# Kernel optimization log

Measured on AMD Instinct MI355X. Metric: run time of the kernel, lower is better.

The kernel has to match this reference:

```python
import jax, jax.numpy as jnp
import numpy as np

DIM = 1024
DEPTH = 6
HEADS = 16
MLP = 4096
HEAD_DIM = DIM // HEADS
SCALE = HEAD_DIM ** -0.5
EPS = 1e-5


def _ln(x, g, b):
    m = jnp.mean(x, axis=-1, keepdims=True)
    v = jnp.mean(jnp.square(x - m), axis=-1, keepdims=True)
    return (x - m) * jax.lax.rsqrt(v + EPS) * g + b


def setup_inputs() -> dict:
    key = jax.random.key(0)
    ks = jax.random.split(key, 16)
    B, N = 4, 1024
    s_d = 1.0 / np.sqrt(DIM)
    s_m = 1.0 / np.sqrt(MLP)
    inp = {
        "x1": jax.random.normal(ks[0], (B, N, DIM), jnp.float32),
        "x2": jax.random.normal(ks[1], (B, N, DIM), jnp.float32),
        # stacked per-layer params; Linear weights stored as [in, out]
        "ln1_g": jnp.ones((DEPTH, DIM), jnp.float32),
        "ln1_b": jnp.zeros((DEPTH, DIM), jnp.float32),
        "wq": jax.random.normal(ks[2], (DEPTH, DIM, DIM), jnp.float32) * s_d,
        "wk": jax.random.normal(ks[3], (DEPTH, DIM, DIM), jnp.float32) * s_d,
        "wv": jax.random.normal(ks[4], (DEPTH, DIM, DIM), jnp.float32) * s_d,
        "wo": jax.random.normal(ks[5], (DEPTH, DIM, DIM), jnp.float32) * s_d,
        "bo": jnp.zeros((DEPTH, DIM), jnp.float32),
        "ln2_g": jnp.ones((DEPTH, DIM), jnp.float32),
        "ln2_b": jnp.zeros((DEPTH, DIM), jnp.float32),
        "w1": jax.random.normal(ks[6], (DEPTH, DIM, MLP), jnp.float32) * s_d,
        "b1": jnp.zeros((DEPTH, MLP), jnp.float32),
        "w2": jax.random.normal(ks[7], (DEPTH, MLP, DIM), jnp.float32) * s_m,
        "b2": jnp.zeros((DEPTH, DIM), jnp.float32),
    }
    return inp


def _split_heads(t):
    b, n, _ = t.shape
    return t.reshape(b, n, HEADS, HEAD_DIM).transpose(0, 2, 1, 3)  # b h n d


def reference(x1, x2, ln1_g, ln1_b, wq, wk, wv, wo, bo, ln2_g, ln2_b, w1, b1, w2, b2):
    # dropout disabled (eval mode)
    for i in range(DEPTH):
        # PreNorm(MCA): same LayerNorm params applied to x1 and x2
        n1 = _ln(x1, ln1_g[i], ln1_b[i])
        n2 = _ln(x2, ln1_g[i], ln1_b[i])
        q = _split_heads(n1 @ wq[i])
        k = _split_heads(n2 @ wk[i])
        v = _split_heads(n2 @ wv[i])
        dots = jnp.einsum('bhqd,bhkd->bhqk', q, k) * SCALE
        attn = jax.nn.softmax(dots, axis=-1)
        out = jnp.einsum('bhqk,bhkd->bhqd', attn, v)
        b, h, n, d = out.shape
        out = out.transpose(0, 2, 1, 3).reshape(b, n, h * d)
        x1 = out @ wo[i] + bo[i] + x1
        # PreNorm(FeedForward)
        nf = _ln(x1, ln2_g[i], ln2_b[i])
        hdn = jax.nn.gelu(nf @ w1[i] + b1[i], approximate=False)
        x1 = hdn @ w2[i] + b2[i] + x1
    return x1
```

## Files before the change

### kernel.cpp

```cpp
#include <hip/hip_runtime.h>
#include <stdint.h>

#define N_SEQ 1024
#define N_TOK 4096
#define ATT_SCALE 0.125f

typedef unsigned short u16;
typedef __attribute__((ext_vector_type(8))) short short8;
typedef __attribute__((ext_vector_type(4))) short short4v;
typedef __attribute__((ext_vector_type(4))) float f32x4;

__device__ __forceinline__ u16 f2bf(float f) {
  uint32_t u = __float_as_uint(f);
  u += 0x7fffu + ((u >> 16) & 1u);
  return (u16)(u >> 16);
}

__device__ __forceinline__ void gload16(const void* g, void* lds) {
  __builtin_amdgcn_global_load_lds(
      (const __attribute__((address_space(1))) unsigned int*)g,
      (__attribute__((address_space(3))) unsigned int*)lds, 16, 0, 0);
}

__global__ void copy_f32_kernel(const float* __restrict__ in, float* __restrict__ out) {
  int i = blockIdx.x * 256 + threadIdx.x;
  ((float4*)out)[i] = ((const float4*)in)[i];
}

__global__ __launch_bounds__(256) void tconv_kernel(const float* __restrict__ src,
                                                    u16* __restrict__ dst,
                                                    int K, int NN, size_t dstLS) {
  __shared__ u16 tile[64][68];
  int n0 = blockIdx.x * 64, k0 = blockIdx.y * 64, L = blockIdx.z;
  const float* s = src + (size_t)L * K * NN;
  u16* d = dst + (size_t)L * dstLS;
  int t = threadIdx.x;
  int rr = t >> 4, cc = (t & 15) * 4;
#pragma unroll
  for (int ii = 0; ii < 4; ii++) {
    int kl = rr + ii * 16;
    float4 v = *(const float4*)&s[(size_t)(k0 + kl) * NN + n0 + cc];
    tile[cc + 0][kl] = f2bf(v.x);
    tile[cc + 1][kl] = f2bf(v.y);
    tile[cc + 2][kl] = f2bf(v.z);
    tile[cc + 3][kl] = f2bf(v.w);
  }
  __syncthreads();
#pragma unroll
  for (int ii = 0; ii < 4; ii++) {
    int nl = rr + ii * 16;
    short4v o;
    o.x = (short)tile[nl][cc + 0];
    o.y = (short)tile[nl][cc + 1];
    o.z = (short)tile[nl][cc + 2];
    o.w = (short)tile[nl][cc + 3];
    *(short4v*)&d[(size_t)(n0 + nl) * K + k0 + cc] = o;
  }
}

__global__ __launch_bounds__(256) void ln_kernel(const float* __restrict__ x,
                                                 const float* __restrict__ g,
                                                 const float* __restrict__ b,
                                                 u16* __restrict__ out) {
  int row = blockIdx.x;
  const float* xr = x + (size_t)row * 1024;
  int t = threadIdx.x;
  float4 v = *(const float4*)&xr[t * 4];
  float s = v.x + v.y + v.z + v.w;
  float sq = v.x * v.x + v.y * v.y + v.z * v.z + v.w * v.w;
#pragma unroll
  for (int m = 1; m < 64; m <<= 1) {
    s += __shfl_xor(s, m, 64);
    sq += __shfl_xor(sq, m, 64);
  }
  __shared__ float ps[8];
  int w = t >> 6;
  if ((t & 63) == 0) { ps[w] = s; ps[4 + w] = sq; }
  __syncthreads();
  s = ps[0] + ps[1] + ps[2] + ps[3];
  sq = ps[4] + ps[5] + ps[6] + ps[7];
  float mean = s * (1.0f / 1024.0f);
  float var = sq * (1.0f / 1024.0f) - mean * mean;
  float rs = rsqrtf(var + 1e-5f);
  float4 gv = *(const float4*)&g[t * 4];
  float4 bv = *(const float4*)&b[t * 4];
  short4v o;
  o.x = (short)f2bf((v.x - mean) * rs * gv.x + bv.x);
  o.y = (short)f2bf((v.y - mean) * rs * gv.y + bv.y);
  o.z = (short)f2bf((v.z - mean) * rs * gv.z + bv.z);
  o.w = (short)f2bf((v.w - mean) * rs * gv.w + bv.w);
  *(short4v*)&out[(size_t)row * 1024 + t * 4] = o;
}

template <int BM, int BN, int WM, int WN, int BK, int D, int MODE>
__global__ __launch_bounds__(WM * WN * 64, 2) void gemmP(const u16* __restrict__ A,
                                                         const u16* __restrict__ Bt,
                                                         u16* __restrict__ outb,
                                                         float* __restrict__ outf,
                                                         const float* __restrict__ bias,
                                                         const float* __restrict__ resid,
                                                         int N, int K) {
  static_assert(BK == 64, "swizzle assumes 8 x 16B chunks per row");
  constexpr int NW = WM * WN;
  constexpr int T = NW * 64;
  constexpr int WTM = BM / WM, WTN = BN / WN;
  constexpr int FM = WTM / 16, FN = WTN / 16;
  constexpr int AT = BM * BK, BTL = BN * BK;
  constexpr int LA = AT / 8 / T, LB = BTL / 8 / T;
  constexpr int LTOT = LA + LB;
  constexpr int WAITN = (D - 1) * LTOT;
  __shared__ u16 smem[D * (AT + BTL)];

  int t = threadIdx.x, lane = t & 63, w = t >> 6;
  int wm = w / WN, wn = w % WN;
  const u16* Ag = A + (size_t)(blockIdx.y * BM) * K;
  const u16* Bg = Bt + (size_t)(blockIdx.x * BN) * K;
  f32x4 acc[FM][FN] = {};

  auto stage = [&](int d, int k0) {
    u16* ab = smem + d * (AT + BTL);
    u16* bb = ab + AT;
#pragma unroll
    for (int l = 0; l < LA; l++) {
      int c = (l * NW + w) * 64 + lane;
      int r = c >> 3, s = c & 7;
      gload16(Ag + (size_t)r * K + k0 + ((s ^ (r & 7)) << 3), ab + (l * NW + w) * 512);
    }
#pragma unroll
    for (int l = 0; l < LB; l++) {
      int c = (l * NW + w) * 64 + lane;
      int r = c >> 3, s = c & 7;
      gload16(Bg + (size_t)r * K + k0 + ((s ^ (r & 7)) << 3), bb + (l * NW + w) * 512);
    }
  };

  const int NT = K / BK;
#pragma unroll
  for (int d = 0; d < D; d++) stage(d, d * BK);
  __builtin_amdgcn_sched_barrier(0);

  int buf = 0;
  for (int tt = 0; tt < NT; tt++) {
    asm volatile("s_waitcnt vmcnt(%0)" ::"n"(WAITN) : "memory");
    __builtin_amdgcn_s_barrier();
    __builtin_amdgcn_sched_barrier(0);
    const u16* ab = smem + buf * (AT + BTL);
    const u16* bb = ab + AT;
    short8 af[2][FM], bfr[2][FN];
#pragma unroll
    for (int ks = 0; ks < 2; ks++) {
      int j = ks * 4 + (lane >> 4);
#pragma unroll
      for (int mi = 0; mi < FM; mi++) {
        int rr = wm * WTM + mi * 16 + (lane & 15);
        af[ks][mi] = *(const short8*)&ab[rr * BK + ((j ^ (rr & 7)) << 3)];
      }
#pragma unroll
      for (int ni = 0; ni < FN; ni++) {
        int rr = wn * WTN + ni * 16 + (lane & 15);
        bfr[ks][ni] = *(const short8*)&bb[rr * BK + ((j ^ (rr & 7)) << 3)];
      }
    }
    asm volatile("s_waitcnt lgkmcnt(0)" ::: "memory");
    __builtin_amdgcn_sched_barrier(0);
    __builtin_amdgcn_s_barrier();
    __builtin_amdgcn_sched_barrier(0);
    stage(buf, ((tt + D) % NT) * BK);
    __builtin_amdgcn_sched_barrier(0);
#pragma unroll
    for (int ks = 0; ks < 2; ks++)
#pragma unroll
      for (int mi = 0; mi < FM; mi++)
#pragma unroll
        for (int ni = 0; ni < FN; ni++)
          acc[mi][ni] = __builtin_amdgcn_mfma_f32_16x16x32_bf16(af[ks][mi], bfr[ks][ni],
                                                                acc[mi][ni], 0, 0, 0);
    buf = (buf + 1 == D) ? 0 : buf + 1;
  }

  int r0 = blockIdx.y * BM + wm * WTM + ((lane >> 4) << 2);
  int c0 = blockIdx.x * BN + wn * WTN + (lane & 15);
#pragma unroll
  for (int mi = 0; mi < FM; mi++) {
#pragma unroll
    for (int r = 0; r < 4; r++) {
      size_t row = (size_t)(r0 + mi * 16 + r);
#pragma unroll
      for (int ni = 0; ni < FN; ni++) {
        size_t col = (size_t)(c0 + ni * 16);
        size_t idx = row * N + col;
        float val = acc[mi][ni][r];
        if (MODE == 0) {
          outb[idx] = f2bf(val);
        } else if (MODE == 1) {
          outf[idx] = val + bias[col] + resid[idx];
        } else {
          float xg = val + bias[col];
          outb[idx] = f2bf(0.5f * xg * (1.0f + erff(xg * 0.70710678f)));
        }
      }
    }
  }
}

__global__ __launch_bounds__(256) void attn_kernel(const u16* __restrict__ qb,
                                                   const u16* __restrict__ kvb,
                                                   u16* __restrict__ ob) {
  int qt = blockIdx.x, bh = blockIdx.y;
  int b = bh >> 4, h = bh & 15;
  int t = threadIdx.x, lane = t & 63, w = t >> 6;
  __shared__ u16 Qs[64 * 64];
  __shared__ u16 Ks[64 * 64];
  __shared__ u16 Vt[64 * 64];
  __shared__ u16 Ps[4][16 * 64];

  const u16* qbase = qb + (size_t)b * N_SEQ * 1024 + h * 64;
  const u16* kbase = kvb + (size_t)b * N_SEQ * 2048 + h * 64;
  const u16* vbase = kbase + 1024;
  u16* obase = ob + (size_t)b * N_SEQ * 1024 + h * 64;

  {
    int r = t >> 2, c = (t & 3) * 16;
    const u16* src = qbase + (size_t)(qt * 64 + r) * 1024 + c;
    *(short8*)&Qs[r * 64 + c] = *(const short8*)src;
    *(short8*)&Qs[r * 64 + c + 8] = *(const short8*)(src + 8);
  }
  __syncthreads();
  short8 qa0 = *(const short8*)&Qs[(w * 16 + (lane & 15)) * 64 + (lane >> 4) * 8];
  short8 qa1 = *(const short8*)&Qs[(w * 16 + (lane & 15)) * 64 + 32 + (lane >> 4) * 8];

  f32x4 o[4] = {};
  float m_r[4] = {-1e30f, -1e30f, -1e30f, -1e30f};
  float l_r[4] = {0.0f, 0.0f, 0.0f, 0.0f};

  for (int kt = 0; kt < 16; kt++) {
    __syncthreads();
    {
      int r = t >> 2, c = (t & 3) * 16;
      const u16* ksrc = kbase + (size_t)(kt * 64 + r) * 2048 + c;
      *(short8*)&Ks[r * 64 + c] = *(const short8*)ksrc;
      *(short8*)&Ks[r * 64 + c + 8] = *(const short8*)(ksrc + 8);
      const u16* vsrc = vbase + (size_t)(kt * 64 + r) * 2048 + c;
      short8 v0 = *(const short8*)vsrc;
      short8 v1 = *(const short8*)(vsrc + 8);
#pragma unroll
      for (int j = 0; j < 8; j++) {
        Vt[(c + j) * 64 + r] = (u16)v0[j];
        Vt[(c + 8 + j) * 64 + r] = (u16)v1[j];
      }
    }
    __syncthreads();

    f32x4 s[4] = {};
#pragma unroll
    for (int kb = 0; kb < 4; kb++) {
      short8 k0 = *(const short8*)&Ks[(kb * 16 + (lane & 15)) * 64 + (lane >> 4) * 8];
      short8 k1 = *(const short8*)&Ks[(kb * 16 + (lane & 15)) * 64 + 32 + (lane >> 4) * 8];
      s[kb] = __builtin_amdgcn_mfma_f32_16x16x32_bf16(qa0, k0, s[kb], 0, 0, 0);
      s[kb] = __builtin_amdgcn_mfma_f32_16x16x32_bf16(qa1, k1, s[kb], 0, 0, 0);
    }
    float fac[4], rowsum[4];
#pragma unroll
    for (int r = 0; r < 4; r++) {
      float a = fmaxf(fmaxf(s[0][r], s[1][r]), fmaxf(s[2][r], s[3][r])) * ATT_SCALE;
      a = fmaxf(a, __shfl_xor(a, 1, 64));
      a = fmaxf(a, __shfl_xor(a, 2, 64));
      a = fmaxf(a, __shfl_xor(a, 4, 64));
      a = fmaxf(a, __shfl_xor(a, 8, 64));
      float mn = fmaxf(m_r[r], a);
      fac[r] = __expf(m_r[r] - mn);
      m_r[r] = mn;
      rowsum[r] = 0.0f;
    }
#pragma unroll
    for (int kb = 0; kb < 4; kb++) {
#pragma unroll
      for (int r = 0; r < 4; r++) {
        float p = __expf(s[kb][r] * ATT_SCALE - m_r[r]);
        rowsum[r] += p;
        Ps[w][((lane >> 4) * 4 + r) * 64 + kb * 16 + (lane & 15)] = f2bf(p);
      }
    }
#pragma unroll
    for (int r = 0; r < 4; r++) {
      float rs = rowsum[r];
      rs += __shfl_xor(rs, 1, 64);
      rs += __shfl_xor(rs, 2, 64);
      rs += __shfl_xor(rs, 4, 64);
      rs += __shfl_xor(rs, 8, 64);
      l_r[r] = l_r[r] * fac[r] + rs;
      o[0][r] *= fac[r];
      o[1][r] *= fac[r];
      o[2][r] *= fac[r];
      o[3][r] *= fac[r];
    }
    __syncthreads();
#pragma unroll
    for (int ks = 0; ks < 2; ks++) {
      short8 pf = *(const short8*)&Ps[w][(lane & 15) * 64 + ks * 32 + (lane >> 4) * 8];
#pragma unroll
      for (int db = 0; db < 4; db++) {
        short8 vf = *(const short8*)&Vt[(db * 16 + (lane & 15)) * 64 + ks * 32 + (lane >> 4) * 8];
        o[db] = __builtin_amdgcn_mfma_f32_16x16x32_bf16(pf, vf, o[db], 0, 0, 0);
      }
    }
  }
#pragma unroll
  for (int r = 0; r < 4; r++) {
    float inv = 1.0f / l_r[r];
    size_t row = (size_t)(qt * 64 + w * 16 + (lane >> 4) * 4 + r);
#pragma unroll
    for (int db = 0; db < 4; db++)
      obase[row * 1024 + db * 16 + (lane & 15)] = f2bf(o[db][r] * inv);
  }
}

extern "C" void kernel_launch(void* const* d_in, const int* in_sizes, int n_in,
                              void* d_out, int out_size, void* d_ws, size_t ws_size,
                              hipStream_t stream) {
  const float* x1 = (const float*)d_in[0];
  const float* x2 = (const float*)d_in[1];
  const float* ln1_g = (const float*)d_in[2];
  const float* ln1_b = (const float*)d_in[3];
  const float* wq = (const float*)d_in[4];
  const float* wk = (const float*)d_in[5];
  const float* wv = (const float*)d_in[6];
  const float* wo = (const float*)d_in[7];
  const float* bo = (const float*)d_in[8];
  const float* ln2_g = (const float*)d_in[9];
  const float* ln2_b = (const float*)d_in[10];
  const float* w1 = (const float*)d_in[11];
  const float* b1 = (const float*)d_in[12];
  const float* w2 = (const float*)d_in[13];
  const float* b2 = (const float*)d_in[14];
  float* xout = (float*)d_out;

  u16* p = (u16*)d_ws;
  u16* wqt = p;  p += (size_t)6 * 1024 * 1024;
  u16* kvt = p;  p += (size_t)6 * 2048 * 1024;
  u16* wot = p;  p += (size_t)6 * 1024 * 1024;
  u16* w1t = p;  p += (size_t)6 * 4096 * 1024;
  u16* w2t = p;  p += (size_t)6 * 1024 * 4096;
  u16* n1 = p;   p += (size_t)N_TOK * 1024;
  u16* n2 = p;   p += (size_t)N_TOK * 1024;
  u16* qbuf = p; p += (size_t)N_TOK * 1024;
  u16* kvbuf = p; p += (size_t)N_TOK * 2048;
  u16* ao = p;   p += (size_t)N_TOK * 1024;
  u16* hid = p;  p += (size_t)N_TOK * 4096;

  dim3 blk(256);
  tconv_kernel<<<dim3(16, 16, 6), blk, 0, stream>>>(wq, wqt, 1024, 1024, (size_t)1024 * 1024);
  tconv_kernel<<<dim3(16, 16, 6), blk, 0, stream>>>(wk, kvt, 1024, 1024, (size_t)2048 * 1024);
  tconv_kernel<<<dim3(16, 16, 6), blk, 0, stream>>>(wv, kvt + (size_t)1024 * 1024, 1024, 1024, (size_t)2048 * 1024);
  tconv_kernel<<<dim3(16, 16, 6), blk, 0, stream>>>(wo, wot, 1024, 1024, (size_t)1024 * 1024);
  tconv_kernel<<<dim3(64, 16, 6), blk, 0, stream>>>(w1, w1t, 1024, 4096, (size_t)4096 * 1024);
  tconv_kernel<<<dim3(16, 64, 6), blk, 0, stream>>>(w2, w2t, 4096, 1024, (size_t)1024 * 4096);
  copy_f32_kernel<<<4096, blk, 0, stream>>>(x1, xout);

  for (int i = 0; i < 6; i++) {
    ln_kernel<<<N_TOK, blk, 0, stream>>>(xout, ln1_g + i * 1024, ln1_b + i * 1024, n1);
    ln_kernel<<<N_TOK, blk, 0, stream>>>(x2, ln1_g + i * 1024, ln1_b + i * 1024, n2);
    gemmP<128, 128, 4, 2, 64, 3, 0><<<dim3(8, 32), dim3(512), 0, stream>>>(
        n1, wqt + (size_t)i * 1024 * 1024, qbuf, nullptr, nullptr, nullptr, 1024, 1024);
    gemmP<128, 128, 2, 2, 64, 2, 0><<<dim3(16, 32), dim3(256), 0, stream>>>(
        n2, kvt + (size_t)i * 2048 * 1024, kvbuf, nullptr, nullptr, nullptr, 2048, 1024);
    attn_kernel<<<dim3(16, 64), blk, 0, stream>>>(qbuf, kvbuf, ao);
    gemmP<128, 128, 4, 2, 64, 3, 1><<<dim3(8, 32), dim3(512), 0, stream>>>(
        ao, wot + (size_t)i * 1024 * 1024, nullptr, xout, bo + i * 1024, xout, 1024, 1024);
    ln_kernel<<<N_TOK, blk, 0, stream>>>(xout, ln2_g + i * 1024, ln2_b + i * 1024, n1);
    gemmP<128, 128, 2, 2, 64, 2, 2><<<dim3(32, 32), dim3(256), 0, stream>>>(
        n1, w1t + (size_t)i * 4096 * 1024, hid, nullptr, b1 + i * 4096, nullptr, 4096, 1024);
    gemmP<128, 128, 4, 2, 64, 3, 1><<<dim3(8, 32), dim3(512), 0, stream>>>(
        hid, w2t + (size_t)i * 1024 * 4096, nullptr, xout, b2 + i * 1024, xout, 1024, 4096);
  }
}
```

Baseline: 1.721 ms.

## Interleave LDS fragment reads with MFMA in fixed double-buffered GEMM

Replaces the configurable-depth GEMM with a fixed two-stage double-buffered kernel. Within each K tile, LDS fragment reads are split into halves and interleaved with MFMA groups, using partial lgkmcnt waits and s_setprio to raise priority during matrix ops. Part of the math now runs after the next global-to-LDS stage is issued. Launch configs also change: most GEMMs drop to 4 waves, and the FFN-up GEMM uses 256x256 tiles with 8 waves. This trades prefetch depth and occupancy for better overlap of LDS latency with compute, and adds register pressure.

```diff
diff --git a/kernel.cpp b/kernel.cpp
--- a/kernel.cpp
+++ b/kernel.cpp
@@ -92,24 +92,23 @@
   *(short4v*)&out[(size_t)row * 1024 + t * 4] = o;
 }
 
-template <int BM, int BN, int WM, int WN, int BK, int D, int MODE>
-__global__ __launch_bounds__(WM * WN * 64, 2) void gemmP(const u16* __restrict__ A,
+template <int BM, int BN, int WM, int WN, int MODE>
+__global__ __launch_bounds__(WM * WN * 64, 2) void gemm8(const u16* __restrict__ A,
                                                          const u16* __restrict__ Bt,
                                                          u16* __restrict__ outb,
                                                          float* __restrict__ outf,
                                                          const float* __restrict__ bias,
                                                          const float* __restrict__ resid,
                                                          int N, int K) {
-  static_assert(BK == 64, "swizzle assumes 8 x 16B chunks per row");
+  constexpr int BK = 64;
   constexpr int NW = WM * WN;
   constexpr int T = NW * 64;
   constexpr int WTM = BM / WM, WTN = BN / WN;
-  constexpr int FM = WTM / 16, FN = WTN / 16;
+  constexpr int FM = WTM / 16, FN = WTN / 16, HM = FM / 2;
   constexpr int AT = BM * BK, BTL = BN * BK;
   constexpr int LA = AT / 8 / T, LB = BTL / 8 / T;
   constexpr int LTOT = LA + LB;
-  constexpr int WAITN = (D - 1) * LTOT;
-  __shared__ u16 smem[D * (AT + BTL)];
+  __shared__ u16 smem[2 * (AT + BTL)];
 
   int t = threadIdx.x, lane = t & 63, w = t >> 6;
   int wm = w / WN, wn = w % WN;
@@ -134,48 +133,83 @@
     }
   };
 
+  auto rdA = [&](const u16* ab, int mi, int ks) {
+    int rr = wm * WTM + mi * 16 + (lane & 15);
+    int j = ks * 4 + (lane >> 4);
+    return *(const short8*)&ab[rr * BK + ((j ^ (rr & 7)) << 3)];
+  };
+  auto rdB = [&](const u16* bb, int ni, int ks) {
+    int rr = wn * WTN + ni * 16 + (lane & 15);
+    int j = ks * 4 + (lane >> 4);
+    return *(const short8*)&bb[rr * BK + ((j ^ (rr & 7)) << 3)];
+  };
+
   const int NT = K / BK;
-#pragma unroll
-  for (int d = 0; d < D; d++) stage(d, d * BK);
+  stage(0, 0);
+  stage(1, BK);
   __builtin_amdgcn_sched_barrier(0);
 
   int buf = 0;
   for (int tt = 0; tt < NT; tt++) {
-    asm volatile("s_waitcnt vmcnt(%0)" ::"n"(WAITN) : "memory");
+    asm volatile("s_waitcnt vmcnt(%0)" ::"n"(LTOT) : "memory");
     __builtin_amdgcn_s_barrier();
     __builtin_amdgcn_sched_barrier(0);
     const u16* ab = smem + buf * (AT + BTL);
     const u16* bb = ab + AT;
-    short8 af[2][FM], bfr[2][FN];
-#pragma unroll
-    for (int ks = 0; ks < 2; ks++) {
-      int j = ks * 4 + (lane >> 4);
-#pragma unroll
-      for (int mi = 0; mi < FM; mi++) {
-        int rr = wm * WTM + mi * 16 + (lane & 15);
-        af[ks][mi] = *(const short8*)&ab[rr * BK + ((j ^ (rr & 7)) << 3)];
-      }
-#pragma unroll
-      for (int ni = 0; ni < FN; ni++) {
-        int rr = wn * WTN + ni * 16 + (lane & 15);
-        bfr[ks][ni] = *(const short8*)&bb[rr * BK + ((j ^ (rr & 7)) << 3)];
-      }
-    }
+    short8 b0[FN], a0lo[HM], a0hi[HM], b1[FN], a1lo[HM], a1hi[HM];
+#pragma unroll
+    for (int n = 0; n < FN; n++) b0[n] = rdB(bb, n, 0);
+#pragma unroll
+    for (int m = 0; m < HM; m++) a0lo[m] = rdA(ab, m, 0);
+#pragma unroll
+    for (int m = 0; m < HM; m++) a0hi[m] = rdA(ab, HM + m, 0);
+    asm volatile("s_waitcnt lgkmcnt(%0)" ::"n"(HM) : "memory");
+    __builtin_amdgcn_sched_barrier(0);
+#pragma unroll
+    for (int n = 0; n < FN; n++) b1[n] = rdB(bb, n, 1);
+#pragma unroll
+    for (int m = 0; m < HM; m++) a1lo[m] = rdA(ab, m, 1);
+    __builtin_amdgcn_s_setprio(1);
+#pragma unroll
+    for (int m = 0; m < HM; m++)
+#pragma unroll
+      for (int n = 0; n < FN; n++)
+        acc[m][n] = __builtin_amdgcn_mfma_f32_16x16x32_bf16(a0lo[m], b0[n], acc[m][n], 0, 0, 0);
+    __builtin_amdgcn_s_setprio(0);
+    asm volatile("s_waitcnt lgkmcnt(%0)" ::"n"(FN + HM) : "memory");
+    __builtin_amdgcn_sched_barrier(0);
+#pragma unroll
+    for (int m = 0; m < HM; m++) a1hi[m] = rdA(ab, HM + m, 1);
+    __builtin_amdgcn_s_setprio(1);
+#pragma unroll
+    for (int m = 0; m < HM; m++)
+#pragma unroll
+      for (int n = 0; n < FN; n++)
+        acc[HM + m][n] = __builtin_amdgcn_mfma_f32_16x16x32_bf16(a0hi[m], b0[n], acc[HM + m][n], 0, 0, 0);
+    __builtin_amdgcn_s_setprio(0);
+    asm volatile("s_waitcnt lgkmcnt(%0)" ::"n"(HM) : "memory");
+    __builtin_amdgcn_sched_barrier(0);
+    __builtin_amdgcn_s_setprio(1);
+#pragma unroll
+    for (int m = 0; m < HM; m++)
+#pragma unroll
+      for (int n = 0; n < FN; n++)
+        acc[m][n] = __builtin_amdgcn_mfma_f32_16x16x32_bf16(a1lo[m], b1[n], acc[m][n], 0, 0, 0);
+    __builtin_amdgcn_s_setprio(0);
     asm volatile("s_waitcnt lgkmcnt(0)" ::: "memory");
     __builtin_amdgcn_sched_barrier(0);
     __builtin_amdgcn_s_barrier();
     __builtin_amdgcn_sched_barrier(0);
-    stage(buf, ((tt + D) % NT) * BK);
-    __builtin_amdgcn_sched_barrier(0);
-#pragma unroll
-    for (int ks = 0; ks < 2; ks++)
-#pragma unroll
-      for (int mi = 0; mi < FM; mi++)
-#pragma unroll
-        for (int ni = 0; ni < FN; ni++)
-          acc[mi][ni] = __builtin_amdgcn_mfma_f32_16x16x32_bf16(af[ks][mi], bfr[ks][ni],
-                                                                acc[mi][ni], 0, 0, 0);
-    buf = (buf + 1 == D) ? 0 : buf + 1;
+    stage(buf, ((tt + 2) % NT) * BK);
+    __builtin_amdgcn_sched_barrier(0);
+    __builtin_amdgcn_s_setprio(1);
+#pragma unroll
+    for (int m = 0; m < HM; m++)
+#pragma unroll
+      for (int n = 0; n < FN; n++)
+        acc[HM + m][n] = __builtin_amdgcn_mfma_f32_16x16x32_bf16(a1hi[m], b1[n], acc[HM + m][n], 0, 0, 0);
+    __builtin_amdgcn_s_setprio(0);
+    buf ^= 1;
   }
 
   int r0 = blockIdx.y * BM + wm * WTM + ((lane >> 4) << 2);
@@ -360,17 +394,17 @@
   for (int i = 0; i < 6; i++) {
     ln_kernel<<<N_TOK, blk, 0, stream>>>(xout, ln1_g + i * 1024, ln1_b + i * 1024, n1);
     ln_kernel<<<N_TOK, blk, 0, stream>>>(x2, ln1_g + i * 1024, ln1_b + i * 1024, n2);
-    gemmP<128, 128, 4, 2, 64, 3, 0><<<dim3(8, 32), dim3(512), 0, stream>>>(
+    gemm8<128, 128, 2, 2, 0><<<dim3(8, 32), dim3(256), 0, stream>>>(
         n1, wqt + (size_t)i * 1024 * 1024, qbuf, nullptr, nullptr, nullptr, 1024, 1024);
-    gemmP<128, 128, 2, 2, 64, 2, 0><<<dim3(16, 32), dim3(256), 0, stream>>>(
+    gemm8<128, 128, 2, 2, 0><<<dim3(16, 32), dim3(256), 0, stream>>>(
         n2, kvt + (size_t)i * 2048 * 1024, kvbuf, nullptr, nullptr, nullptr, 2048, 1024);
     attn_kernel<<<dim3(16, 64), blk, 0, stream>>>(qbuf, kvbuf, ao);
-    gemmP<128, 128, 4, 2, 64, 3, 1><<<dim3(8, 32), dim3(512), 0, stream>>>(
+    gemm8<128, 128, 2, 2, 1><<<dim3(8, 32), dim3(256), 0, stream>>>(
         ao, wot + (size_t)i * 1024 * 1024, nullptr, xout, bo + i * 1024, xout, 1024, 1024);
     ln_kernel<<<N_TOK, blk, 0, stream>>>(xout, ln2_g + i * 1024, ln2_b + i * 1024, n1);
-    gemmP<128, 128, 2, 2, 64, 2, 2><<<dim3(32, 32), dim3(256), 0, stream>>>(
+    gemm8<256, 256, 2, 4, 2><<<dim3(16, 16), dim3(512), 0, stream>>>(
         n1, w1t + (size_t)i * 4096 * 1024, hid, nullptr, b1 + i * 4096, nullptr, 4096, 1024);
-    gemmP<128, 128, 4, 2, 64, 3, 1><<<dim3(8, 32), dim3(512), 0, stream>>>(
+    gemm8<128, 128, 2, 2, 1><<<dim3(8, 32), dim3(256), 0, stream>>>(
         hid, w2t + (size_t)i * 1024 * 4096, nullptr, xout, b2 + i * 1024, xout, 1024, 4096);
   }
 }
```

Measured after the change: 1.823 ms. 1.06x slower.
